# Optimization experiments

Measured on AMD Instinct MI355X. Metric: run time of the kernel, lower is better.

Reference implementation:

```python
import jax, jax.numpy as jnp
import numpy as np

V_TH = 0.5       # heaviside threshold (HeavisideBoxcar forward = hard step)
OUT_TAU = 0.96   # init_tau used for the output LIF node
STDP_LR = 0.01
STDP_W = 3       # stdp_time_window


def setup_inputs() -> dict:
    key = jax.random.key(0)
    ks = jax.random.split(key, 6)
    n_in, H, n_out, T = 1024, 4096, 256, 128
    # batch must be 1: original code does spike_history[:, -1] = hidden_spike.squeeze()
    x = jax.random.uniform(ks[0], (1, T, n_in), dtype=jnp.float32)
    w_fc1 = jax.random.uniform(ks[1], (H, n_in), minval=-1.0, maxval=1.0, dtype=jnp.float32) / np.float32(np.sqrt(n_in))
    w_out = jax.random.uniform(ks[2], (n_out, H), minval=-1.0, maxval=1.0, dtype=jnp.float32) / np.float32(np.sqrt(H))
    recurrent = jax.random.uniform(ks[3], (H, H), dtype=jnp.float32) / np.float32(np.sqrt(H))
    tau_hidden = (0.96 - 0.02) + 0.04 * jax.random.uniform(ks[4], (H,), dtype=jnp.float32)
    mask = jnp.ones((H, H), jnp.float32) - jnp.eye(H, dtype=jnp.float32)  # no self-connections
    binary = (jax.random.uniform(ks[5], (H, H)) > 0.3).astype(jnp.float32)
    return {"x": x, "w_fc1": w_fc1, "w_out": w_out, "recurrent": recurrent,
            "tau_hidden": tau_hidden, "mask": mask, "binary": binary}


def reference(x, w_fc1, w_out, recurrent, tau_hidden, mask, binary):
    B, T, _ = x.shape
    H = recurrent.shape[0]
    n_out = w_out.shape[0]
    # effective recurrent weights are frozen for the whole forward pass
    eff_rec = recurrent * mask * binary                 # [H, H]
    ff = jnp.einsum('bti,hi->bth', x, w_fc1)            # precomputed feedforward drive [B, T, H]

    def step(carry, ff_t):
        h_mem, h_spk, o_mem, o_spk, hist, rec = carry
        cur_h = ff_t + 0.1 * (h_spk @ eff_rec)          # [B, H]
        h_mem = h_mem * tau_hidden * (1.0 - h_spk) + cur_h
        h_spk = (h_mem >= V_TH).astype(h_mem.dtype)
        o_mem = o_mem * OUT_TAU * (1.0 - o_spk) + h_spk @ w_out.T
        o_spk = (o_mem >= V_TH).astype(o_mem.dtype)
        # roll spike history left and append current hidden spikes (batch == 1)
        hist = jnp.concatenate([hist[:, 1:], h_spk[0][:, None]], axis=1)   # [H, STDP_W]
        # STDP: per window slot t, +lr where hist[i,t] - cur[j] <= 0 else -lr
        diff = hist[:, :, None] - h_spk[0][None, None, :]                  # [H, STDP_W, H]
        count = jnp.sum(diff <= 0.0, axis=1).astype(rec.dtype)             # [H, H]
        rec = rec + STDP_LR * (2.0 * count - STDP_W)
        return (h_mem, h_spk, o_mem, o_spk, hist, rec), o_spk

    init = (jnp.zeros((B, H), x.dtype), jnp.zeros((B, H), x.dtype),
            jnp.zeros((B, n_out), x.dtype), jnp.zeros((B, n_out), x.dtype),
            jnp.zeros((H, STDP_W), x.dtype), recurrent)
    carry, outs = jax.lax.scan(step, init, jnp.swapaxes(ff, 0, 1))
    # outputs [B, T, n_out] plus the STDP-updated recurrent weights (side effect in torch)
    return jnp.swapaxes(outs, 0, 1), carry[5]
```

## Files before the change

### kernel.cpp

```cpp
#include <hip/hip_runtime.h>
#include <cstdint>
#include <cstddef>

#define HN    4096
#define TT    128
#define NIN   1024
#define NOUTC 256
#define NWGH  64
#define NWGO  4
#define NWGT  (NWGH + NWGO)
#define NRB   64
#define S_A   5

__global__ __launch_bounds__(256) void k_pre(
    const float4* __restrict__ r4,
    const float4* __restrict__ b4, float4* __restrict__ e4,
    double* __restrict__ colP, unsigned* __restrict__ zbase, int zwords)
{
    const int chunk = blockIdx.x;
    const int band  = blockIdx.y;
    const int tid   = threadIdx.x;
    if (chunk == 0 && band == 0) {
        for (int i = tid; i < zwords; i += 256) zbase[i] = 0u;
    }
    const int col4 = chunk * 256 + tid;
    double a0 = 0.0, a1 = 0.0, a2 = 0.0, a3 = 0.0;
    for (int r = 0; r < 64; ++r) {
        const int row = band * 64 + r;
        const size_t idx = (size_t)row * (HN / 4) + col4;
        float4 a = r4[idx], c = b4[idx];
        float4 o;
        o.x = a.x * c.x;
        o.y = a.y * c.y;
        o.z = a.z * c.z;
        o.w = a.w * c.w;
        if (col4 == (row >> 2)) {
            const int comp = row & 3;
            if      (comp == 0) o.x = 0.f;
            else if (comp == 1) o.y = 0.f;
            else if (comp == 2) o.z = 0.f;
            else                o.w = 0.f;
        }
        e4[idx] = o;
        a0 += (double)o.x; a1 += (double)o.y; a2 += (double)o.z; a3 += (double)o.w;
    }
    double* cp = colP + (size_t)band * HN + (size_t)col4 * 4;
    cp[0] = a0; cp[1] = a1; cp[2] = a2; cp[3] = a3;
}

__global__ __launch_bounds__(256) void k_misc(const float* __restrict__ wout,
                                              float* __restrict__ wT,
                                              double* __restrict__ colvO)
{
    const int bx = blockIdx.x;
    if (bx < 256) {
        __shared__ float tile[64][65];
        const int h0 = (bx & 63) * 64;
        const int o0 = (bx >> 6) * 64;
        const int lx = threadIdx.x & 63, ly = threadIdx.x >> 6;
        #pragma unroll
        for (int i = 0; i < 16; ++i) {
            int o = ly + 4 * i;
            tile[o][lx] = wout[(size_t)(o0 + o) * HN + h0 + lx];
        }
        __syncthreads();
        #pragma unroll
        for (int i = 0; i < 16; ++i) {
            int h = ly + 4 * i;
            wT[(size_t)(h0 + h) * NOUTC + o0 + lx] = tile[lx][h];
        }
    } else {
        const int b2 = bx - 256;
        const int wv = threadIdx.x >> 6, lane = threadIdx.x & 63;
        const int o = b2 * 4 + wv;
        double s = 0.0;
        const float* p = wout + (size_t)o * HN + lane;
        #pragma unroll 8
        for (int j = 0; j < 64; ++j) s += (double)p[(size_t)j * 64];
        #pragma unroll
        for (int d = 1; d < 64; d <<= 1) {
            union { double d2; long long l; } u; u.d2 = s;
            u.l = __shfl_xor(u.l, d, 64);
            s += u.d2;
        }
        if (lane == 0) colvO[o] = s;
    }
}

__global__ __launch_bounds__(256) void k_ff(const float* __restrict__ x,
                                            const float* __restrict__ w,
                                            double* __restrict__ ff)
{
    __shared__ float xs[16][36];
    __shared__ float wsT[32][73];
    const int h0 = blockIdx.x * 64;
    const int t0 = blockIdx.y * 16;
    const int tid = threadIdx.x;
    const int tq = tid >> 5, hq = tid & 31;
    double acc00 = 0.0, acc01 = 0.0, acc10 = 0.0, acc11 = 0.0;
    for (int kc = 0; kc < NIN; kc += 32) {
        __syncthreads();
        #pragma unroll
        for (int s2 = 0; s2 < 2; ++s2) {
            int e = tid + s2 * 256; int t = e >> 5, k = e & 31;
            xs[t][k] = x[(size_t)(t0 + t) * NIN + kc + k];
        }
        #pragma unroll
        for (int s2 = 0; s2 < 8; ++s2) {
            int e = tid + s2 * 256; int h = e >> 5, k = e & 31;
            wsT[k][h] = w[(size_t)(h0 + h) * NIN + kc + k];
        }
        __syncthreads();
        #pragma unroll 8
        for (int k = 0; k < 32; ++k) {
            double a0 = (double)xs[tq][k];
            double a1 = (double)xs[tq + 8][k];
            double b0 = (double)wsT[k][hq];
            double b1 = (double)wsT[k][hq + 32];
            acc00 += a0 * b0; acc01 += a0 * b1;
            acc10 += a1 * b0; acc11 += a1 * b1;
        }
    }
    ff[(size_t)(t0 + tq) * HN + h0 + hq]          = acc00;
    ff[(size_t)(t0 + tq) * HN + h0 + hq + 32]     = acc01;
    ff[(size_t)(t0 + tq + 8) * HN + h0 + hq]      = acc10;
    ff[(size_t)(t0 + tq + 8) * HN + h0 + hq + 32] = acc11;
}

__global__ __launch_bounds__(256) void k_colred(const double* __restrict__ colP,
                                                double* __restrict__ colvH)
{
    const int h = blockIdx.x * 256 + threadIdx.x;
    double s = 0.0;
    #pragma unroll
    for (int rb = 0; rb < NRB; ++rb) s += colP[(size_t)rb * HN + h];
    colvH[h] = s;
}

__global__ __launch_bounds__(256) void k_sat(const double* __restrict__ ff,
                                             const double* __restrict__ colvH,
                                             unsigned* __restrict__ satFail)
{
    __shared__ int s_ok[4];
    const int t = S_A + blockIdx.x;
    const int tid = threadIdx.x;
    bool ok = true;
    #pragma unroll
    for (int i = 0; i < 16; ++i) {
        const int h = tid + 256 * i;
        ok = ok && ((ff[(size_t)t * HN + h] + 0.1 * colvH[h]) >= 0.5);
    }
    unsigned long long b = __ballot(ok);
    if ((tid & 63) == 0) s_ok[tid >> 6] = (b == ~0ULL) ? 1 : 0;
    __syncthreads();
    if (tid == 0) {
        if (!(s_ok[0] & s_ok[1] & s_ok[2] & s_ok[3])) atomicOr(satFail, 1u);
    }
}

__global__ __launch_bounds__(1024) void k_loopA(
    const float* __restrict__ eff, const float* __restrict__ wT,
    const double* __restrict__ ff, const float* __restrict__ tau,
    const double* __restrict__ colvH, const double* __restrict__ colvO,
    unsigned long long* spk, unsigned long long* bar, float* out,
    double* __restrict__ hmS, unsigned* __restrict__ flagsS,
    unsigned* __restrict__ AS, unsigned* __restrict__ N0S, unsigned* __restrict__ N1S,
    double* __restrict__ omS, unsigned* __restrict__ oflagsS)
{
    __shared__ unsigned short s_list[2048];
    __shared__ double s_part[16][64];
    __shared__ int s_kbc;

    const int wg = blockIdx.x;
    const int tid = threadIdx.x;
    const int wv = tid >> 6;
    const int lane = tid & 63;
    const bool isH = (wg < NWGH);

    const size_t rstride = isH ? (size_t)HN : (size_t)NOUTC;
    const int base0 = isH ? wg * 64 : (wg - NWGH) * 64;
    const float* gbase = (isH ? eff : wT) + base0 + lane;
    const int c = base0 + lane;

    double colv = 0.0, hm = 0.0, om = 0.0, ffv = 0.0;
    float tauv = 0.f;
    int sp1 = 0, sp2 = 0, osp = 0;
    unsigned curA = 0, curN0 = 0, curN1 = 0, naccr = 0;
    if (wv == 0) {
        if (isH) { colv = colvH[c]; tauv = tau[c]; ffv = ff[c]; }
        else     { colv = colvO[c]; }
    }
    unsigned lsense = 0;
    int kcur = 0;
    unsigned myCnt = 0;

    for (int it = 0; it <= S_A; ++it) {
        const bool active = isH ? (it < S_A) : (it > 0);
        if (active) {
            const int k = kcur;
            const bool gspk = (k <= HN / 2);
            const int nlist = gspk ? k : HN - k;
            if (nlist > 0) {
                if (tid < 64) {
                    unsigned long long w = __hip_atomic_load(
                        &spk[(size_t)((it + 1) & 1) * 64 + lane],
                        __ATOMIC_RELAXED, __HIP_MEMORY_SCOPE_AGENT);
                    unsigned long long myw = gspk ? w : ~w;
                    int cnt = __popcll(myw);
                    int incl = cnt;
                    #pragma unroll
                    for (int d = 1; d < 64; d <<= 1) {
                        int o = __shfl_up(incl, d, 64);
                        if (lane >= d) incl += o;
                    }
                    int b = incl - cnt;
                    while (myw) {
                        int bp = __builtin_ctzll(myw);
                        s_list[b++] = (unsigned short)(lane * 64 + bp);
                        myw &= myw - 1;
                    }
                }
                __syncthreads();
                double acc = 0.0;
                int idx = wv;
                for (; idx + 112 < nlist; idx += 128) {
                    const float v0 = gbase[(size_t)s_list[idx      ] * rstride];
                    const float v1 = gbase[(size_t)s_list[idx + 16 ] * rstride];
                    const float v2 = gbase[(size_t)s_list[idx + 32 ] * rstride];
                    const float v3 = gbase[(size_t)s_list[idx + 48 ] * rstride];
                    const float v4 = gbase[(size_t)s_list[idx + 64 ] * rstride];
                    const float v5 = gbase[(size_t)s_list[idx + 80 ] * rstride];
                    const float v6 = gbase[(size_t)s_list[idx + 96 ] * rstride];
                    const float v7 = gbase[(size_t)s_list[idx + 112] * rstride];
                    acc += (((double)v0 + (double)v1) + ((double)v2 + (double)v3))
                         + (((double)v4 + (double)v5) + ((double)v6 + (double)v7));
                }
                for (; idx < nlist; idx += 16)
                    acc += (double)gbase[(size_t)s_list[idx] * rstride];
                s_part[wv][lane] = acc;
                __syncthreads();
            }
            if (wv == 0) {
                double ssum = 0.0;
                if (nlist > 0) {
                    #pragma unroll
                    for (int p = 0; p < 16; ++p) ssum += s_part[p][lane];
                }
                double drive = gspk ? ssum : (colv - ssum);
                if (isH) {
                    const int t = it;
                    double cur = ffv + 0.1 * drive;
                    hm = hm * (double)tauv * (double)(1 - sp1) + cur;
                    int s = (hm >= 0.5) ? 1 : 0;
                    int n = s + sp1 + sp2;
                    sp2 = sp1; sp1 = s;
                    naccr += (unsigned)n;
                    unsigned bit = 1u << (t & 31);
                    if (s)     curA  |= bit;
                    if (n & 1) curN0 |= bit;
                    if (n & 2) curN1 |= bit;
                    unsigned long long ball = __ballot(s != 0);
                    if (lane == 0) {
                        __hip_atomic_store(&spk[(size_t)(t & 1) * 64 + wg], ball,
                                           __ATOMIC_RELEASE, __HIP_MEMORY_SCOPE_AGENT);
                        __threadfence();
                        myCnt = (unsigned)__popcll(ball);
                    }
                    ffv = ff[(size_t)(it + 1) * HN + c];
                } else {
                    const int t = it - 1;
                    om = om * 0.96 * (double)(1 - osp) + drive;
                    osp = (om >= 0.5) ? 1 : 0;
                    out[(size_t)t * NOUTC + c] = osp ? 1.0f : 0.0f;
                }
            }
        }
        if (it < S_A) {
            __syncthreads();
            if (tid == 0) {
                unsigned s = lsense ^ 1u;
                lsense = s;
                unsigned cntW = isH ? myCnt : 0u;
                unsigned long long prev = __hip_atomic_fetch_add(
                    &bar[0], (1ULL << 32) + (unsigned long long)cntW,
                    __ATOMIC_ACQ_REL, __HIP_MEMORY_SCOPE_AGENT);
                unsigned long long v;
                if ((unsigned)(prev >> 32) == NWGT - 1u) {
                    unsigned ktot = (unsigned)(prev & 0xffffffffULL) + cntW;
                    __hip_atomic_store(&bar[0], 0ULL, __ATOMIC_RELAXED, __HIP_MEMORY_SCOPE_AGENT);
                    v = ((unsigned long long)ktot << 1) | (unsigned long long)s;
                    __hip_atomic_store(&bar[1], v, __ATOMIC_RELEASE, __HIP_MEMORY_SCOPE_AGENT);
                } else {
                    int budget = 1 << 17;
                    for (;;) {
                        v = __hip_atomic_load(&bar[1], __ATOMIC_ACQUIRE, __HIP_MEMORY_SCOPE_AGENT);
                        if ((unsigned)(v & 1ULL) == s) break;
                        if (--budget == 0) break;
                    }
                }
                s_kbc = (int)(v >> 1);
            }
            __syncthreads();
            kcur = s_kbc;
        }
    }
    if (wv == 0) {
        if (isH) {
            hmS[c] = hm;
            flagsS[c] = (unsigned)sp1 | ((unsigned)sp2 << 1) | (naccr << 2);
            AS[c] = curA; N0S[c] = curN0; N1S[c] = curN1;
        } else {
            omS[c] = om;
            oflagsS[c] = (unsigned)osp;
        }
    }
}

__global__ __launch_bounds__(1024) void k_loopB(
    const float* __restrict__ eff, const float* __restrict__ wT,
    const double* __restrict__ ff, const float* __restrict__ tau,
    const double* __restrict__ colvH, const double* __restrict__ colvO,
    const unsigned long long* __restrict__ spk,
    const double* __restrict__ hmS, const unsigned* __restrict__ flagsS,
    const unsigned* __restrict__ AS, const unsigned* __restrict__ N0S,
    const unsigned* __restrict__ N1S,
    const double* __restrict__ omS, const unsigned* __restrict__ oflagsS,
    const unsigned* __restrict__ satFail,
    unsigned* __restrict__ AwP, unsigned* __restrict__ N0wP,
    unsigned* __restrict__ N1wP, unsigned* __restrict__ Nacc,
    float* __restrict__ out)
{
    __shared__ unsigned long long s_words[64];
    __shared__ unsigned short s_list[2048];

    const int tid = threadIdx.x;
    const int wv = tid >> 6, lane = tid & 63;

    double hm[4], colv[4], tauv[4];
    unsigned curA[4], curN0[4], curN1[4], nacc[4];
    int sp1[4], sp2[4];
    #pragma unroll
    for (int p = 0; p < 4; ++p) {
        const int c = tid + 1024 * p;
        hm[p] = hmS[c];
        unsigned f = flagsS[c];
        sp1[p] = f & 1; sp2[p] = (f >> 1) & 1; nacc[p] = f >> 2;
        curA[p] = AS[c]; curN0[p] = N0S[c]; curN1[p] = N1S[c];
        tauv[p] = (double)tau[c];
        colv[p] = colvH[c];
    }
    double om = 0.0, colO = 0.0;
    int osp = 0;
    if (tid < NOUTC) {
        om = omS[tid]; osp = (int)(oflagsS[tid] & 1u);
        colO = colvO[tid];
    }

    if (tid < 64) s_words[tid] = spk[(size_t)((S_A - 1) & 1) * 64 + tid];
    __syncthreads();
    int kprev;
    {
        int v = __popcll(s_words[lane]);
        #pragma unroll
        for (int d = 1; d < 64; d <<= 1) v += __shfl_xor(v, d, 64);
        kprev = v;
    }
    bool gprev = (kprev <= HN / 2);
    int nprev = gprev ? kprev : HN - kprev;
    const bool satOK = (satFail[0] == 0u);
    bool allspike = (kprev == HN);

    if (nprev > 0) {
        if (tid < 64) {
            unsigned long long myw = gprev ? s_words[tid] : ~s_words[tid];
            int cnt = __popcll(myw), incl = cnt;
            #pragma unroll
            for (int d = 1; d < 64; d <<= 1) { int o = __shfl_up(incl, d, 64); if (lane >= d) incl += o; }
            int b = incl - cnt;
            while (myw) { int bp = __builtin_ctzll(myw); s_list[b++] = (unsigned short)(tid * 64 + bp); myw &= myw - 1; }
        }
        __syncthreads();
    }

    int t = S_A;
    while (t < TT && !(satOK && allspike)) {
        double fcur[4];
        #pragma unroll
        for (int p = 0; p < 4; ++p) fcur[p] = ff[(size_t)t * HN + tid + 1024 * p];
        double drv[4];
        if (nprev > 0) {
            double s0 = 0.0, s1 = 0.0, s2 = 0.0, s3 = 0.0;
            for (int idx = 0; idx < nprev; ++idx) {
                const float* rp = eff + (size_t)s_list[idx] * HN + tid;
                s0 += (double)rp[0];
                s1 += (double)rp[1024];
                s2 += (double)rp[2048];
                s3 += (double)rp[3072];
            }
            drv[0] = gprev ? s0 : (colv[0] - s0);
            drv[1] = gprev ? s1 : (colv[1] - s1);
            drv[2] = gprev ? s2 : (colv[2] - s2);
            drv[3] = gprev ? s3 : (colv[3] - s3);
        } else {
            #pragma unroll
            for (int p = 0; p < 4; ++p) drv[p] = gprev ? 0.0 : colv[p];
        }
        int sb[4];
        const unsigned bit = 1u << (t & 31);
        #pragma unroll
        for (int p = 0; p < 4; ++p) {
            double cur = fcur[p] + 0.1 * drv[p];
            hm[p] = hm[p] * tauv[p] * (double)(1 - sp1[p]) + cur;
            sb[p] = (hm[p] >= 0.5) ? 1 : 0;
            int n = sb[p] + sp1[p] + sp2[p];
            sp2[p] = sp1[p]; sp1[p] = sb[p];
            nacc[p] += (unsigned)n;
            if (sb[p]) curA[p] |= bit;
            if (n & 1) curN0[p] |= bit;
            if (n & 2) curN1[p] |= bit;
        }
        if ((t & 31) == 31) {
            const int wq = t >> 5;
            #pragma unroll
            for (int p = 0; p < 4; ++p) {
                const int c = tid + 1024 * p;
                AwP [wq * HN + c] = curA[p];
                N0wP[wq * HN + c] = curN0[p];
                N1wP[wq * HN + c] = curN1[p];
                curA[p] = curN0[p] = curN1[p] = 0u;
            }
        }
        __syncthreads();
        #pragma unroll
        for (int p = 0; p < 4; ++p) {
            unsigned long long b = __ballot(sb[p] != 0);
            if (lane == 0) s_words[16 * p + wv] = b;
        }
        __syncthreads();
        int k;
        {
            int v = __popcll(s_words[lane]);
            #pragma unroll
            for (int d = 1; d < 64; d <<= 1) v += __shfl_xor(v, d, 64);
            k = v;
        }
        const bool gspk = (k <= HN / 2);
        const int nlist = gspk ? k : HN - k;
        if (nlist > 0) {
            if (tid < 64) {
                unsigned long long myw = gspk ? s_words[tid] : ~s_words[tid];
                int cnt = __popcll(myw), incl = cnt;
                #pragma unroll
                for (int d = 1; d < 64; d <<= 1) { int o = __shfl_up(incl, d, 64); if (lane >= d) incl += o; }
                int b2 = incl - cnt;
                while (myw) { int bp = __builtin_ctzll(myw); s_list[b2++] = (unsigned short)(tid * 64 + bp); myw &= myw - 1; }
            }
            __syncthreads();
        }
        if (tid < NOUTC) {
            double so = 0.0;
            for (int idx = 0; idx < nlist; ++idx)
                so += (double)wT[(size_t)s_list[idx] * NOUTC + tid];
            double drv_o = gspk ? so : (colO - so);
            om = om * 0.96 * (double)(1 - osp) + drv_o;
            osp = (om >= 0.5) ? 1 : 0;
            out[(size_t)t * NOUTC + tid] = osp ? 1.0f : 0.0f;
        }
        gprev = gspk; nprev = nlist;
        allspike = (k == HN);
        ++t;
    }

    if (t < TT) {
        const int t_sw = t;
        const int wq_sw = t_sw >> 5;
        const int off = t_sw & 31;
        const unsigned hiA = 0xFFFFFFFFu << off;
        const unsigned hi1 = (off < 31) ? (0xFFFFFFFFu << (off + 1)) : 0u;
        #pragma unroll
        for (int p = 0; p < 4; ++p) {
            const int c = tid + 1024 * p;
            AwP [wq_sw * HN + c] = curA[p]  | hiA;
            N0wP[wq_sw * HN + c] = curN0[p] | ((unsigned)sp2[p] << off) | hi1;
            N1wP[wq_sw * HN + c] = curN1[p] | hiA;
            for (int wq = wq_sw + 1; wq < 4; ++wq) {
                AwP [wq * HN + c] = 0xFFFFFFFFu;
                N0wP[wq * HN + c] = 0xFFFFFFFFu;
                N1wP[wq * HN + c] = 0xFFFFFFFFu;
            }
            Nacc[c] = nacc[p] + (unsigned)(2 + sp2[p]) + 3u * (unsigned)(TT - 1 - t_sw);
        }
        if (tid < NOUTC) {
            for (int tt = t_sw; tt < TT; ++tt) {
                om = om * 0.96 * (double)(1 - osp) + colO;
                osp = (om >= 0.5) ? 1 : 0;
                out[(size_t)tt * NOUTC + tid] = osp ? 1.0f : 0.0f;
            }
        }
        return;
    }
    #pragma unroll
    for (int p = 0; p < 4; ++p) Nacc[tid + 1024 * p] = nacc[p];
}

__global__ __launch_bounds__(256) void k_rec(const float* __restrict__ recur,
    const unsigned* __restrict__ AwP, const unsigned* __restrict__ N0wP,
    const unsigned* __restrict__ N1wP, const unsigned* __restrict__ Nacc,
    float* __restrict__ out)
{
    const int j = blockIdx.x * 256 + threadIdx.x;
    const int i0 = blockIdx.y * 32;
    const unsigned a0 = AwP[0 * HN + j], a1 = AwP[1 * HN + j];
    const unsigned a2 = AwP[2 * HN + j], a3 = AwP[3 * HN + j];
    for (int ii = 0; ii < 32; ++ii) {
        const int i = i0 + ii;
        const unsigned n00 = N0wP[0 * HN + i], n01 = N0wP[1 * HN + i];
        const unsigned n02 = N0wP[2 * HN + i], n03 = N0wP[3 * HN + i];
        const unsigned n10 = N1wP[0 * HN + i], n11 = N1wP[1 * HN + i];
        const unsigned n12 = N1wP[2 * HN + i], n13 = N1wP[3 * HN + i];
        int M = __popc(a0 & n00) + __popc(a1 & n01) + __popc(a2 & n02) + __popc(a3 & n03);
        M += 2 * (__popc(a0 & n10) + __popc(a1 & n11) + __popc(a2 & n12) + __popc(a3 & n13));
        const int D = 3 * TT - 2 * (int)Nacc[i] + 2 * M;
        out[(size_t)i * HN + j] = (float)((double)recur[(size_t)i * HN + j] + 0.01 * (double)D);
    }
}

extern "C" void kernel_launch(void* const* d_in, const int* in_sizes, int n_in,
                              void* d_out, int out_size, void* d_ws, size_t ws_size,
                              hipStream_t stream) {
    const float* x         = (const float*)d_in[0];
    const float* w_fc1     = (const float*)d_in[1];
    const float* w_out     = (const float*)d_in[2];
    const float* recurrent = (const float*)d_in[3];
    const float* tau       = (const float*)d_in[4];
    const float* binary    = (const float*)d_in[6];
    float* out = (float*)d_out;
    float* rec_out = out + (size_t)TT * NOUTC;
    float* eff = rec_out;

    char* ws = (char*)d_ws;
    size_t off = 0;
    float* wT  = (float*)(ws + off);                 off += (size_t)HN * NOUTC * 4;
    double* ff = (double*)(ws + off);                off += (size_t)TT * HN * 8;
    unsigned long long* spk = (unsigned long long*)(ws + off); off += 2 * 64 * 8;
    unsigned long long* bar = (unsigned long long*)(ws + off); off += 256;
    unsigned* satFail = (unsigned*)((char*)bar + 128);
    const int zwords = (int)((2 * 64 * 8 + 256) / 4);
    unsigned* AwP  = (unsigned*)(ws + off);          off += (size_t)4 * HN * 4;
    unsigned* N0wP = (unsigned*)(ws + off);          off += (size_t)4 * HN * 4;
    unsigned* N1wP = (unsigned*)(ws + off);          off += (size_t)4 * HN * 4;
    unsigned* Nacc = (unsigned*)(ws + off);          off += (size_t)HN * 4;
    double* colP   = (double*)(ws + off);            off += (size_t)NRB * HN * 8;
    double* colvH  = (double*)(ws + off);            off += (size_t)HN * 8;
    double* colvO  = (double*)(ws + off);            off += (size_t)NOUTC * 8;
    double*   hmS    = (double*)(ws + off);          off += (size_t)HN * 8;
    unsigned* flagsS = (unsigned*)(ws + off);        off += (size_t)HN * 4;
    unsigned* AS     = (unsigned*)(ws + off);        off += (size_t)HN * 4;
    unsigned* N0S    = (unsigned*)(ws + off);        off += (size_t)HN * 4;
    unsigned* N1S    = (unsigned*)(ws + off);        off += (size_t)HN * 4;
    double*   omS    = (double*)(ws + off);          off += (size_t)NOUTC * 8;
    unsigned* oflagsS= (unsigned*)(ws + off);        off += (size_t)NOUTC * 4;

    if (ws_size < off) return;

    k_pre<<<dim3(4, 64), dim3(256), 0, stream>>>(
        (const float4*)recurrent, (const float4*)binary,
        (float4*)eff, colP, (unsigned*)spk, zwords);
    k_misc<<<dim3(320), dim3(256), 0, stream>>>(w_out, wT, colvO);
    k_ff<<<dim3(64, 8), dim3(256), 0, stream>>>(x, w_fc1, ff);
    k_colred<<<dim3(16), dim3(256), 0, stream>>>(colP, colvH);
    k_sat<<<dim3(TT - S_A), dim3(256), 0, stream>>>(ff, colvH, satFail);
    k_loopA<<<dim3(NWGT), dim3(1024), 0, stream>>>(eff, wT, ff, tau, colvH, colvO,
                                                   spk, bar, out,
                                                   hmS, flagsS, AS, N0S, N1S, omS, oflagsS);
    k_loopB<<<dim3(1), dim3(1024), 0, stream>>>(eff, wT, ff, tau, colvH, colvO, spk,
                                                hmS, flagsS, AS, N0S, N1S, omS, oflagsS,
                                                satFail, AwP, N0wP, N1wP, Nacc, out);
    k_rec<<<dim3(16, 128), dim3(256), 0, stream>>>(recurrent, AwP, N0wP, N1wP, Nacc,
                                                   rec_out);
}
```

Before: 211.2 us.

## Use hierarchical two-level grid barrier and batch loads in preprocessing kernel

Replaces the single global atomic counter in the persistent kernel's grid barrier with a two-level tree. Workgroups first arrive at one of eight group counters on separate cache lines, and group leaders then combine spike counts at a top-level counter and broadcast the result per group. This is meant to cut atomic contention on one address among 68 workgroups at each early barrier, at the cost of an extra atomic round trip on the critical path. The preprocessing kernel also issues four rows of loads before computing, which should improve memory-level parallelism.

```diff
diff --git a/kernel.cpp b/kernel.cpp
--- a/kernel.cpp
+++ b/kernel.cpp
@@ -25,24 +25,34 @@
     }
     const int col4 = chunk * 256 + tid;
     double a0 = 0.0, a1 = 0.0, a2 = 0.0, a3 = 0.0;
-    for (int r = 0; r < 64; ++r) {
-        const int row = band * 64 + r;
-        const size_t idx = (size_t)row * (HN / 4) + col4;
-        float4 a = r4[idx], c = b4[idx];
-        float4 o;
-        o.x = a.x * c.x;
-        o.y = a.y * c.y;
-        o.z = a.z * c.z;
-        o.w = a.w * c.w;
-        if (col4 == (row >> 2)) {
-            const int comp = row & 3;
-            if      (comp == 0) o.x = 0.f;
-            else if (comp == 1) o.y = 0.f;
-            else if (comp == 2) o.z = 0.f;
-            else                o.w = 0.f;
-        }
-        e4[idx] = o;
-        a0 += (double)o.x; a1 += (double)o.y; a2 += (double)o.z; a3 += (double)o.w;
+    for (int rb = 0; rb < 64; rb += 4) {
+        float4 av[4], cv[4];
+        size_t idxs[4];
+        #pragma unroll
+        for (int j = 0; j < 4; ++j) {
+            const int row = band * 64 + rb + j;
+            idxs[j] = (size_t)row * (HN / 4) + col4;
+            av[j] = r4[idxs[j]];
+            cv[j] = b4[idxs[j]];
+        }
+        #pragma unroll
+        for (int j = 0; j < 4; ++j) {
+            const int row = band * 64 + rb + j;
+            float4 o;
+            o.x = av[j].x * cv[j].x;
+            o.y = av[j].y * cv[j].y;
+            o.z = av[j].z * cv[j].z;
+            o.w = av[j].w * cv[j].w;
+            if (col4 == (row >> 2)) {
+                const int comp = row & 3;
+                if      (comp == 0) o.x = 0.f;
+                else if (comp == 1) o.y = 0.f;
+                else if (comp == 2) o.z = 0.f;
+                else                o.w = 0.f;
+            }
+            e4[idxs[j]] = o;
+            a0 += (double)o.x; a1 += (double)o.y; a2 += (double)o.z; a3 += (double)o.w;
+        }
     }
     double* cp = colP + (size_t)band * HN + (size_t)col4 * 4;
     cp[0] = a0; cp[1] = a1; cp[2] = a2; cp[3] = a3;
@@ -280,20 +290,37 @@
             if (tid == 0) {
                 unsigned s = lsense ^ 1u;
                 lsense = s;
-                unsigned cntW = isH ? myCnt : 0u;
+                const int g = wg & 7;
+                const unsigned gsize = (g < 4) ? 9u : 8u;
+                unsigned long long cntW = isH ? (unsigned long long)myCnt : 0ull;
                 unsigned long long prev = __hip_atomic_fetch_add(
-                    &bar[0], (1ULL << 32) + (unsigned long long)cntW,
+                    &bar[g * 8], (1ULL << 32) + cntW,
                     __ATOMIC_ACQ_REL, __HIP_MEMORY_SCOPE_AGENT);
                 unsigned long long v;
-                if ((unsigned)(prev >> 32) == NWGT - 1u) {
-                    unsigned ktot = (unsigned)(prev & 0xffffffffULL) + cntW;
-                    __hip_atomic_store(&bar[0], 0ULL, __ATOMIC_RELAXED, __HIP_MEMORY_SCOPE_AGENT);
-                    v = ((unsigned long long)ktot << 1) | (unsigned long long)s;
-                    __hip_atomic_store(&bar[1], v, __ATOMIC_RELEASE, __HIP_MEMORY_SCOPE_AGENT);
+                if ((unsigned)(prev >> 32) == gsize - 1u) {
+                    unsigned long long ksumg = (prev & 0xffffffffULL) + cntW;
+                    __hip_atomic_store(&bar[g * 8], 0ULL, __ATOMIC_RELAXED, __HIP_MEMORY_SCOPE_AGENT);
+                    unsigned long long pt = __hip_atomic_fetch_add(
+                        &bar[64], (1ULL << 32) + ksumg,
+                        __ATOMIC_ACQ_REL, __HIP_MEMORY_SCOPE_AGENT);
+                    if ((unsigned)(pt >> 32) == 7u) {
+                        unsigned long long ktot = (pt & 0xffffffffULL) + ksumg;
+                        __hip_atomic_store(&bar[64], 0ULL, __ATOMIC_RELAXED, __HIP_MEMORY_SCOPE_AGENT);
+                        v = (ktot << 1) | (unsigned long long)s;
+                        __hip_atomic_store(&bar[72], v, __ATOMIC_RELEASE, __HIP_MEMORY_SCOPE_AGENT);
+                    } else {
+                        int budget = 1 << 17;
+                        for (;;) {
+                            v = __hip_atomic_load(&bar[72], __ATOMIC_ACQUIRE, __HIP_MEMORY_SCOPE_AGENT);
+                            if ((unsigned)(v & 1ULL) == s) break;
+                            if (--budget == 0) break;
+                        }
+                    }
+                    __hip_atomic_store(&bar[80 + g * 8], v, __ATOMIC_RELEASE, __HIP_MEMORY_SCOPE_AGENT);
                 } else {
                     int budget = 1 << 17;
                     for (;;) {
-                        v = __hip_atomic_load(&bar[1], __ATOMIC_ACQUIRE, __HIP_MEMORY_SCOPE_AGENT);
+                        v = __hip_atomic_load(&bar[80 + g * 8], __ATOMIC_ACQUIRE, __HIP_MEMORY_SCOPE_AGENT);
                         if ((unsigned)(v & 1ULL) == s) break;
                         if (--budget == 0) break;
                     }
@@ -543,9 +570,9 @@
     float* wT  = (float*)(ws + off);                 off += (size_t)HN * NOUTC * 4;
     double* ff = (double*)(ws + off);                off += (size_t)TT * HN * 8;
     unsigned long long* spk = (unsigned long long*)(ws + off); off += 2 * 64 * 8;
-    unsigned long long* bar = (unsigned long long*)(ws + off); off += 256;
-    unsigned* satFail = (unsigned*)((char*)bar + 128);
-    const int zwords = (int)((2 * 64 * 8 + 256) / 4);
+    unsigned long long* bar = (unsigned long long*)(ws + off); off += 2048;
+    unsigned* satFail = (unsigned*)((char*)bar + 1280);
+    const int zwords = (int)((2 * 64 * 8 + 2048) / 4);
     unsigned* AwP  = (unsigned*)(ws + off);          off += (size_t)4 * HN * 4;
     unsigned* N0wP = (unsigned*)(ws + off);          off += (size_t)4 * HN * 4;
     unsigned* N1wP = (unsigned*)(ws + off);          off += (size_t)4 * HN * 4;
```

New measurement: 217.1 us. 1.03x slower.
